# Performance work log

Hardware: AMD Instinct MI355X
Metric: run time of the kernel (lower is better)

The kernel has to match this reference:

```python
import jax, jax.numpy as jnp
import numpy as np


def setup_inputs() -> dict:
    key = jax.random.key(0)
    kq, kk, kv = jax.random.split(key, 3)
    b, n, h, d = 1, 8192, 8, 64
    return {
        "query": jax.random.normal(kq, (b, n, h, d), dtype=jnp.float32),
        "key": jax.random.normal(kk, (b, n, h, d), dtype=jnp.float32),
        "value": jax.random.normal(kv, (b, n, h, d), dtype=jnp.float32),
        "ring_size": 4,
    }


def _ring_attention(q, k, v, ring_size):
    # q,k,v: [b, n, h, d]. Emulates the ring: K/V split into ring_size chunks,
    # processed sequentially with online-softmax rescaling (non-causal).
    b, n, h, d = q.shape
    cs = n // ring_size  # chunk_size
    scale = 1.0 / jnp.sqrt(jnp.asarray(d, q.dtype))
    # [ring, b, cs, h, d]
    k_chunks = jnp.moveaxis(k.reshape(b, ring_size, cs, h, d), 1, 0)
    v_chunks = jnp.moveaxis(v.reshape(b, ring_size, cs, h, d), 1, 0)

    out0 = jnp.zeros((b, h, n, d), q.dtype)
    m0 = jnp.full((b, h, n, 1), -jnp.inf, q.dtype)
    s0 = jnp.zeros((b, h, n, 1), q.dtype)

    def step(carry, kv_chunk):
        out, m, s = carry
        kc, vc = kv_chunk  # [b, cs, h, d]
        scores = jnp.einsum("bqhd,bkhd->bhqk", q, kc) * scale  # [b,h,n,cs]
        chunk_max = scores.max(axis=-1, keepdims=True)
        new_max = jnp.maximum(m, chunk_max)
        corr = jnp.exp(m - new_max)  # 0 at first step since m=-inf
        exp_scores = jnp.exp(scores - new_max)
        out = out * corr + jnp.einsum("bhqk,bkhd->bhqd", exp_scores, vc)
        s = s * corr + exp_scores.sum(axis=-1, keepdims=True)
        return (out, new_max, s), None

    (out, _, s), _ = jax.lax.scan(step, (out0, m0, s0), (k_chunks, v_chunks))
    out = out / s
    return jnp.swapaxes(out, 1, 2)  # [b, n, h, d]


def reference(query, key, value, ring_size):
    return _ring_attention(query, key, value, ring_size)
```

## Files before the change

### kernel.cpp

```cpp
#include <hip/hip_runtime.h>
#include <hip/hip_bf16.h>

typedef __attribute__((ext_vector_type(8))) short bf16x8;
typedef __attribute__((ext_vector_type(8))) unsigned short u16x8;
typedef __attribute__((ext_vector_type(16))) float f32x16;
typedef __attribute__((ext_vector_type(4))) unsigned int u32x4;

#define MFMA32(a, b, c) __builtin_amdgcn_mfma_f32_32x32x16_bf16(a, b, c, 0, 0, 0)

constexpr int NSEQ = 8192;
constexpr int NH   = 8;
constexpr int DIM  = 64;
constexpr int KVB  = 64;
constexpr int NT   = NSEQ / KVB;
constexpr int NTH  = NT / 2;
constexpr int SLAB = KVB * DIM;
constexpr int QB   = 256;
constexpr float SCL2 = 0.18033688011112042f;

__device__ __forceinline__ unsigned cvt_pk(float lo, float hi) {
    unsigned r;
    asm("v_cvt_pk_bf16_f32 %0, %1, %2" : "=v"(r) : "v"(lo), "v"(hi));
    return r;
}
__device__ __forceinline__ float exp2f_fast(float x) {
    float r;
    asm("v_exp_f32 %0, %1" : "=v"(r) : "v"(x));
    return r;
}
__device__ __forceinline__ void pl32swap(unsigned& a, unsigned& b) {
    asm("v_permlane32_swap_b32 %0, %1" : "+v"(a), "+v"(b));
}
__device__ __forceinline__ int swz(int row, int col) {
    return row * 64 + ((((col >> 3) ^ row) & 7) << 3) + (col & 7);
}

__global__ __launch_bounds__(256, 4)
void prep_kernel(const float* __restrict__ Kg, const float* __restrict__ Vg,
                 unsigned short* __restrict__ Kws, unsigned short* __restrict__ Vws) {
    __shared__ float Vf[64][65];
    const int tid = threadIdx.x;
    const int bid = blockIdx.x;
    if (bid < 1024) {
        const int h = bid >> 7, t = bid & 127;
        unsigned short* dst = Kws + (size_t)bid * SLAB;
#pragma unroll
        for (int j = 0; j < 2; ++j) {
            const int m = tid * 2 + j;
            const int instr = m >> 6, ln = m & 63;
            const int kh = instr >> 2, kd = instr & 3;
            const int row = t * 64 + kh * 32 + (ln & 31);
            const int col = kd * 16 + (ln >> 5) * 8;
            const float* src = Kg + ((size_t)row * NH + h) * DIM + col;
            float4 a = ((const float4*)src)[0];
            float4 b = ((const float4*)src)[1];
            u32x4 w;
            w[0] = cvt_pk(a.x, a.y); w[1] = cvt_pk(a.z, a.w);
            w[2] = cvt_pk(b.x, b.y); w[3] = cvt_pk(b.z, b.w);
            *(u32x4*)(dst + m * 8) = w;
        }
    } else {
        const int hb = bid - 1024;
        const int h = hb >> 7, t = hb & 127;
        const int key = tid >> 2, dc = (tid & 3) * 16;
        const float* src = Vg + ((size_t)(t * 64 + key) * NH + h) * DIM + dc;
#pragma unroll
        for (int i = 0; i < 4; ++i) {
            float4 a = ((const float4*)src)[i];
            Vf[key][dc + i * 4 + 0] = a.x; Vf[key][dc + i * 4 + 1] = a.y;
            Vf[key][dc + i * 4 + 2] = a.z; Vf[key][dc + i * 4 + 3] = a.w;
        }
        __syncthreads();
        unsigned short* dst = Vws + (size_t)hb * SLAB;
#pragma unroll
        for (int j = 0; j < 2; ++j) {
            const int m = tid * 2 + j;
            const int instr = m >> 6, ln = m & 63;
            const int vh = instr >> 2, ks = instr & 3;
            const int d  = vh * 32 + (ln & 31);
            const int k0 = ks * 16 + (ln >> 5) * 8;
            u32x4 w;
            w[0] = cvt_pk(Vf[k0 + 0][d], Vf[k0 + 1][d]);
            w[1] = cvt_pk(Vf[k0 + 2][d], Vf[k0 + 3][d]);
            w[2] = cvt_pk(Vf[k0 + 4][d], Vf[k0 + 5][d]);
            w[3] = cvt_pk(Vf[k0 + 6][d], Vf[k0 + 7][d]);
            *(u32x4*)(dst + m * 8) = w;
        }
    }
}

__global__ __launch_bounds__(512, 2)
void fa_kernel(const float* __restrict__ Qg, const unsigned short* __restrict__ Kws,
               const unsigned short* __restrict__ Vws, float* __restrict__ Og) {
    __shared__ unsigned short KVb[2][2][2][SLAB];
    __shared__ float mrgML[2][2][256];

    const int tid  = threadIdx.x;
    const int lane = tid & 63;
    const int wave = tid >> 6;
    const int half = wave >> 2;
    const int qw   = wave & 1;
    const int qw2  = (wave >> 1) & 1;
    const int la31 = lane & 31;
    const int hi   = lane >> 5;
    const int halftid = tid & 255;
    const int head  = blockIdx.x & 7;
    const int qtile = blockIdx.x >> 3;
    const int qwv = wave & 3;
    const int qv = wave & 3;
    const int qbase = qtile * 128 + (qv & 1) * 64;
    const int fragoff = lane * 8;

    const int half_f  = wave >> 1;
    const int qv_f    = wave & 1;
    const int qbase_f = qtile * 128 + qv_f * 64;
    const int halftid_f = tid & 127;

    bf16x8 qf[2][4];
#pragma unroll
    for (int g = 0; g < 2; ++g)
#pragma unroll
        for (int kd = 0; kd < 4; ++kd) {
            const float* qp = Qg + ((size_t)(qbase_f + g * 32 + la31) * NH + head) * DIM + kd * 16 + hi * 8;
            float4 a = ((const float4*)qp)[0];
            float4 b = ((const float4*)qp)[1];
            u32x4 w;
            w[0] = cvt_pk(a.x * SCL2, a.y * SCL2);
            w[1] = cvt_pk(a.z * SCL2, a.w * SCL2);
            w[2] = cvt_pk(b.x * SCL2, b.y * SCL2);
            w[3] = cvt_pk(b.z * SCL2, b.w * SCL2);
            qf[g][kd] = __builtin_bit_cast(bf16x8, w);
        }

    const unsigned short* ksl = Kws + ((size_t)head * NT + (size_t)half_f * NTH) * SLAB + halftid_f * 8;
    const unsigned short* vsl = Vws + ((size_t)head * NT + (size_t)half_f * NTH) * SLAB + halftid_f * 8;

    f32x16 oacc[2][2];
#pragma unroll
    for (int g = 0; g < 2; ++g)
#pragma unroll
        for (int nt = 0; nt < 2; ++nt)
#pragma unroll
            for (int i = 0; i < 16; ++i) oacc[g][nt][i] = 0.f;
    float m_run[2] = {-1e30f, -1e30f}, l_run[2] = {0.f, 0.f};

    u16x8 kr0 = *(const u16x8*)ksl,          kr1 = *(const u16x8*)(ksl + 1024);
    u16x8 kr2 = *(const u16x8*)(ksl + 2048), kr3 = *(const u16x8*)(ksl + 3072);
    u16x8 vr0 = *(const u16x8*)vsl,          vr1 = *(const u16x8*)(vsl + 1024);
    u16x8 vr2 = *(const u16x8*)(vsl + 2048), vr3 = *(const u16x8*)(vsl + 3072);
    ksl += SLAB; vsl += SLAB;

    for (int t = 0; t < NTH; ++t) {
        const int cur = t & 1;
        unsigned short* kw = &KVb[0][half_f][cur][0];
        unsigned short* vw = &KVb[1][half_f][cur][0];
        *(u16x8*)(kw + halftid_f * 8)        = kr0;
        *(u16x8*)(kw + 1024 + halftid_f * 8) = kr1;
        *(u16x8*)(kw + 2048 + halftid_f * 8) = kr2;
        *(u16x8*)(kw + 3072 + halftid_f * 8) = kr3;
        *(u16x8*)(vw + halftid_f * 8)        = vr0;
        *(u16x8*)(vw + 1024 + halftid_f * 8) = vr1;
        *(u16x8*)(vw + 2048 + halftid_f * 8) = vr2;
        *(u16x8*)(vw + 3072 + halftid_f * 8) = vr3;
        __syncthreads();
        if (t + 1 < NTH) {
            kr0 = *(const u16x8*)ksl;          kr1 = *(const u16x8*)(ksl + 1024);
            kr2 = *(const u16x8*)(ksl + 2048); kr3 = *(const u16x8*)(ksl + 3072);
            vr0 = *(const u16x8*)vsl;          vr1 = *(const u16x8*)(vsl + 1024);
            vr2 = *(const u16x8*)(vsl + 2048); vr3 = *(const u16x8*)(vsl + 3072);
            ksl += SLAB; vsl += SLAB;
        }
        const unsigned short* Kbase = &KVb[0][half_f][cur][0];
        const unsigned short* Vbase = &KVb[1][half_f][cur][0];

        f32x16 s00, s01, s10, s11;
#pragma unroll
        for (int i = 0; i < 16; ++i) { s00[i] = 0.f; s01[i] = 0.f; s10[i] = 0.f; s11[i] = 0.f; }
        __builtin_amdgcn_s_setprio(1);
#pragma unroll
        for (int kd = 0; kd < 4; ++kd) {
            bf16x8 k0 = *(const bf16x8*)(Kbase + kd * 512 + fragoff);
            bf16x8 k1 = *(const bf16x8*)(Kbase + (4 + kd) * 512 + fragoff);
            s00 = MFMA32(k0, qf[0][kd], s00);
            s01 = MFMA32(k1, qf[0][kd], s01);
            s10 = MFMA32(k0, qf[1][kd], s10);
            s11 = MFMA32(k1, qf[1][kd], s11);
        }
        __builtin_amdgcn_s_setprio(0);

#pragma unroll
        for (int g = 0; g < 2; ++g) {
            const f32x16& a = g ? s10 : s00;
            const f32x16& b = g ? s11 : s01;
            float pmv[16];
#pragma unroll
            for (int i = 0; i < 16; ++i) pmv[i] = fmaxf(a[i], b[i]);
#pragma unroll
            for (int st = 8; st >= 1; st >>= 1)
#pragma unroll
                for (int i = 0; i < 8; ++i)
                    if (i < st) pmv[i] = fmaxf(pmv[i], pmv[i + st]);
            float pm = pmv[0];
            pm = fmaxf(pm, __shfl_xor(pm, 32));
            if (__any(pm > m_run[g] + 8.f)) {
                float mnew = fmaxf(m_run[g], pm);
                float corr = exp2f_fast(m_run[g] - mnew);
                m_run[g] = mnew;
                l_run[g] *= corr;
#pragma unroll
                for (int i = 0; i < 16; ++i) { oacc[g][0][i] *= corr; oacc[g][1][i] *= corr; }
            }
        }

#pragma unroll
        for (int kb = 0; kb < 2; ++kb) {
            bf16x8 frg[2][2];
#pragma unroll
            for (int g = 0; g < 2; ++g) {
                const f32x16& s = g ? (kb ? s11 : s10) : (kb ? s01 : s00);
                float p[16];
#pragma unroll
                for (int i = 0; i < 16; ++i) p[i] = exp2f_fast(s[i] - m_run[g]);
                float ts[8];
#pragma unroll
                for (int i = 0; i < 8; ++i) ts[i] = p[i] + p[i + 8];
#pragma unroll
                for (int i = 0; i < 4; ++i) ts[i] += ts[i + 4];
                l_run[g] += (ts[0] + ts[1]) + (ts[2] + ts[3]);
                unsigned A[8];
#pragma unroll
                for (int j = 0; j < 8; ++j) A[j] = cvt_pk(p[2 * j], p[2 * j + 1]);
                pl32swap(A[0], A[2]); pl32swap(A[1], A[3]);
                pl32swap(A[4], A[6]); pl32swap(A[5], A[7]);
                u32x4 f0v; f0v[0] = A[0]; f0v[1] = A[1]; f0v[2] = A[2]; f0v[3] = A[3];
                u32x4 f1v; f1v[0] = A[4]; f1v[1] = A[5]; f1v[2] = A[6]; f1v[3] = A[7];
                frg[g][0] = __builtin_bit_cast(bf16x8, f0v);
                frg[g][1] = __builtin_bit_cast(bf16x8, f1v);
            }
            __builtin_amdgcn_s_setprio(1);
#pragma unroll
            for (int ks2 = 0; ks2 < 2; ++ks2) {
                const int ksg = kb * 2 + ks2;
                bf16x8 vf0 = *(const bf16x8*)(Vbase + ksg * 512 + fragoff);
                bf16x8 vf1 = *(const bf16x8*)(Vbase + (4 + ksg) * 512 + fragoff);
                oacc[0][0] = MFMA32(vf0, frg[0][ks2], oacc[0][0]);
                oacc[0][1] = MFMA32(vf1, frg[0][ks2], oacc[0][1]);
                oacc[1][0] = MFMA32(vf0, frg[1][ks2], oacc[1][0]);
                oacc[1][1] = MFMA32(vf1, frg[1][ks2], oacc[1][1]);
            }
            __builtin_amdgcn_s_setprio(0);
        }
    }

    __syncthreads();
    float* mrgO = (float*)&KVb[0][0][0][0];
    const int row0 = qv_f * 64;
    if (half_f) {
#pragma unroll
        for (int g = 0; g < 2; ++g) {
            const int row = row0 + g * 32 + la31;
#pragma unroll
            for (int nt = 0; nt < 2; ++nt)
#pragma unroll
                for (int i = 0; i < 16; ++i)
                    mrgO[hi * 4096 + (nt * 16 + i) * 128 + row] = oacc[g][nt][i];
            mrgML[g][0][qv_f * 64 + lane] = m_run[g];
            mrgML[g][1][qv_f * 64 + lane] = l_run[g];
        }
    }
    __syncthreads();
    if (!half_f) {
#pragma unroll
        for (int g = 0; g < 2; ++g) {
            const int row = row0 + g * 32 + la31;
            const float m1 = mrgML[g][0][qv_f * 64 + lane];
            const float l1 = mrgML[g][1][qv_f * 64 + lane];
            const float mnew = fmaxf(m_run[g], m1);
            const float c0 = exp2f_fast(m_run[g] - mnew);
            const float c1 = exp2f_fast(m1 - mnew);
            float lt = l_run[g] * c0 + l1 * c1;
#pragma unroll
            for (int nt = 0; nt < 2; ++nt)
#pragma unroll
                for (int i = 0; i < 16; ++i)
                    oacc[g][nt][i] = oacc[g][nt][i] * c0 + mrgO[hi * 4096 + (nt * 16 + i) * 128 + row] * c1;
            const float l_tot = lt + __shfl_xor(lt, 32);
            const float inv = __builtin_amdgcn_rcpf(l_tot);
            float* obase = Og + ((size_t)(qtile * 128 + row) * NH + head) * DIM;
#pragma unroll
            for (int nt = 0; nt < 2; ++nt)
#pragma unroll
                for (int rq = 0; rq < 4; ++rq) {
                    float4 o;
                    o.x = oacc[g][nt][rq * 4 + 0] * inv;
                    o.y = oacc[g][nt][rq * 4 + 1] * inv;
                    o.z = oacc[g][nt][rq * 4 + 2] * inv;
                    o.w = oacc[g][nt][rq * 4 + 3] * inv;
                    *(float4*)(obase + nt * 32 + rq * 8 + hi * 4) = o;
                }
        }
    }
}

__global__ __launch_bounds__(256, 2)
void fb_kernel(const float* __restrict__ Qg, const float* __restrict__ Kg,
               const float* __restrict__ Vg, float* __restrict__ Og) {
    __shared__ unsigned short Kl[KVB][DIM];
    __shared__ unsigned short Vt[DIM][KVB];
    unsigned short* Kbase = &Kl[0][0];
    unsigned short* Vbase = &Vt[0][0];
    const int tid  = threadIdx.x;
    const int lane = tid & 63;
    const int wave = tid >> 6;
    const int la31 = lane & 31;
    const int hi   = lane >> 5;
    const int head  = blockIdx.x & 7;
    const int qtile = blockIdx.x >> 3;
    const int q     = qtile * 128 + wave * 32 + la31;
    bf16x8 qf[4];
#pragma unroll
    for (int kd = 0; kd < 4; ++kd) {
        const float* qp = Qg + ((size_t)q * NH + head) * DIM + kd * 16 + hi * 8;
        float4 a = ((const float4*)qp)[0];
        float4 b = ((const float4*)qp)[1];
        u32x4 w;
        w[0] = cvt_pk(a.x * SCL2, a.y * SCL2);
        w[1] = cvt_pk(a.z * SCL2, a.w * SCL2);
        w[2] = cvt_pk(b.x * SCL2, b.y * SCL2);
        w[3] = cvt_pk(b.z * SCL2, b.w * SCL2);
        qf[kd] = __builtin_bit_cast(bf16x8, w);
    }
    const int ksrow = tid & 63;
    const int kscol = (tid >> 6) * 16;
    const int vpair = tid & 31;
    const int vcg   = tid >> 5;
    const float* kptr  = Kg + ((size_t)ksrow * NH + head) * DIM + kscol;
    const float* vptr0 = Vg + ((size_t)(2 * vpair) * NH + head) * DIM + vcg * 8;
    const float* vptr1 = vptr0 + NH * DIM;
    constexpr size_t STRIDE = (size_t)KVB * NH * DIM;
    const int kIdx0 = swz(ksrow, kscol);
    const int kIdx1 = swz(ksrow, kscol + 8);
    f32x16 oacc[2];
#pragma unroll
    for (int nt = 0; nt < 2; ++nt)
#pragma unroll
        for (int i = 0; i < 16; ++i) oacc[nt][i] = 0.f;
    float m_run = -1e30f, l_run = 0.f;
    float4 kr0 = ((const float4*)kptr)[0], kr1 = ((const float4*)kptr)[1];
    float4 kr2 = ((const float4*)kptr)[2], kr3 = ((const float4*)kptr)[3];
    float4 va0 = ((const float4*)vptr0)[0], va1 = ((const float4*)vptr0)[1];
    float4 vb0 = ((const float4*)vptr1)[0], vb1 = ((const float4*)vptr1)[1];
    kptr += STRIDE; vptr0 += STRIDE; vptr1 += STRIDE;
    for (int t = 0; t < NT; ++t) {
        __syncthreads();
        {
            u32x4 w;
            w[0] = cvt_pk(kr0.x, kr0.y); w[1] = cvt_pk(kr0.z, kr0.w);
            w[2] = cvt_pk(kr1.x, kr1.y); w[3] = cvt_pk(kr1.z, kr1.w);
            *(u32x4*)(Kbase + kIdx0) = w;
            w[0] = cvt_pk(kr2.x, kr2.y); w[1] = cvt_pk(kr2.z, kr2.w);
            w[2] = cvt_pk(kr3.x, kr3.y); w[3] = cvt_pk(kr3.z, kr3.w);
            *(u32x4*)(Kbase + kIdx1) = w;
        }
        {
            *(unsigned*)(Vbase + swz(vcg * 8 + 0, 2 * vpair)) = cvt_pk(va0.x, vb0.x);
            *(unsigned*)(Vbase + swz(vcg * 8 + 1, 2 * vpair)) = cvt_pk(va0.y, vb0.y);
            *(unsigned*)(Vbase + swz(vcg * 8 + 2, 2 * vpair)) = cvt_pk(va0.z, vb0.z);
            *(unsigned*)(Vbase + swz(vcg * 8 + 3, 2 * vpair)) = cvt_pk(va0.w, vb0.w);
            *(unsigned*)(Vbase + swz(vcg * 8 + 4, 2 * vpair)) = cvt_pk(va1.x, vb1.x);
            *(unsigned*)(Vbase + swz(vcg * 8 + 5, 2 * vpair)) = cvt_pk(va1.y, vb1.y);
            *(unsigned*)(Vbase + swz(vcg * 8 + 6, 2 * vpair)) = cvt_pk(va1.z, vb1.z);
            *(unsigned*)(Vbase + swz(vcg * 8 + 7, 2 * vpair)) = cvt_pk(va1.w, vb1.w);
        }
        __syncthreads();
        if (t + 1 < NT) {
            kr0 = ((const float4*)kptr)[0]; kr1 = ((const float4*)kptr)[1];
            kr2 = ((const float4*)kptr)[2]; kr3 = ((const float4*)kptr)[3];
            va0 = ((const float4*)vptr0)[0]; va1 = ((const float4*)vptr0)[1];
            vb0 = ((const float4*)vptr1)[0]; vb1 = ((const float4*)vptr1)[1];
            kptr += STRIDE; vptr0 += STRIDE; vptr1 += STRIDE;
        }
        f32x16 s0, s1;
#pragma unroll
        for (int i = 0; i < 16; ++i) { s0[i] = 0.f; s1[i] = 0.f; }
        __builtin_amdgcn_s_setprio(1);
#pragma unroll
        for (int kd = 0; kd < 4; ++kd) {
            bf16x8 k0 = *(const bf16x8*)(Kbase + swz(la31, kd * 16 + hi * 8));
            bf16x8 k1 = *(const bf16x8*)(Kbase + swz(32 + la31, kd * 16 + hi * 8));
            s0 = MFMA32(k0, qf[kd], s0);
            s1 = MFMA32(k1, qf[kd], s1);
        }
        __builtin_amdgcn_s_setprio(0);
        float pmv[16];
#pragma unroll
        for (int i = 0; i < 16; ++i) pmv[i] = fmaxf(s0[i], s1[i]);
#pragma unroll
        for (int st = 8; st >= 1; st >>= 1)
#pragma unroll
            for (int i = 0; i < 8; ++i)
                if (i < st) pmv[i] = fmaxf(pmv[i], pmv[i + st]);
        float pm = pmv[0];
        pm = fmaxf(pm, __shfl_xor(pm, 32));
        if (__any(pm > m_run + 8.f)) {
            float mnew = fmaxf(m_run, pm);
            float corr = exp2f_fast(m_run - mnew);
            m_run = mnew;
            l_run *= corr;
#pragma unroll
            for (int i = 0; i < 16; ++i) { oacc[0][i] *= corr; oacc[1][i] *= corr; }
        }
#pragma unroll
        for (int kb = 0; kb < 2; ++kb) {
            const f32x16& s = kb ? s1 : s0;
            float p[16];
#pragma unroll
            for (int i = 0; i < 16; ++i) p[i] = exp2f_fast(s[i] - m_run);
            float ts[8];
#pragma unroll
            for (int i = 0; i < 8; ++i) ts[i] = p[i] + p[i + 8];
#pragma unroll
            for (int i = 0; i < 4; ++i) ts[i] += ts[i + 4];
            l_run += (ts[0] + ts[1]) + (ts[2] + ts[3]);
            unsigned A[8];
#pragma unroll
            for (int j = 0; j < 8; ++j) A[j] = cvt_pk(p[2 * j], p[2 * j + 1]);
            pl32swap(A[0], A[2]); pl32swap(A[1], A[3]);
            pl32swap(A[4], A[6]); pl32swap(A[5], A[7]);
            u32x4 f0v; f0v[0] = A[0]; f0v[1] = A[1]; f0v[2] = A[2]; f0v[3] = A[3];
            u32x4 f1v; f1v[0] = A[4]; f1v[1] = A[5]; f1v[2] = A[6]; f1v[3] = A[7];
            bf16x8 frag[2] = { __builtin_bit_cast(bf16x8, f0v), __builtin_bit_cast(bf16x8, f1v) };
            __builtin_amdgcn_s_setprio(1);
#pragma unroll
            for (int ksl = 0; ksl < 2; ++ksl) {
                const int ksg = kb * 2 + ksl;
                bf16x8 vf0 = *(const bf16x8*)(Vbase + swz(la31, ksg * 16 + hi * 8));
                bf16x8 vf1 = *(const bf16x8*)(Vbase + swz(32 + la31, ksg * 16 + hi * 8));
                oacc[0] = MFMA32(vf0, frag[ksl], oacc[0]);
                oacc[1] = MFMA32(vf1, frag[ksl], oacc[1]);
            }
            __builtin_amdgcn_s_setprio(0);
        }
    }
    {
        float l_tot = l_run + __shfl_xor(l_run, 32);
        float inv = __builtin_amdgcn_rcpf(l_tot);
        float* obase = Og + ((size_t)q * NH + head) * DIM;
#pragma unroll
        for (int nt = 0; nt < 2; ++nt)
#pragma unroll
            for (int rq = 0; rq < 4; ++rq) {
                float4 o;
                o.x = oacc[nt][rq * 4 + 0] * inv;
                o.y = oacc[nt][rq * 4 + 1] * inv;
                o.z = oacc[nt][rq * 4 + 2] * inv;
                o.w = oacc[nt][rq * 4 + 3] * inv;
                *(float4*)(obase + nt * 32 + rq * 8 + hi * 4) = o;
            }
    }
}

extern "C" void kernel_launch(void* const* d_in, const int* in_sizes, int n_in,
                              void* d_out, int out_size, void* d_ws, size_t ws_size,
                              hipStream_t stream) {
    const float* q = (const float*)d_in[0];
    const float* k = (const float*)d_in[1];
    const float* v = (const float*)d_in[2];
    float* out = (float*)d_out;
    constexpr size_t KV_WS = 2ull * NH * NT * SLAB * sizeof(unsigned short);
    if (ws_size >= KV_WS) {
        unsigned short* Kws = (unsigned short*)d_ws;
        unsigned short* Vws = Kws + (size_t)NH * NT * SLAB;
        hipLaunchKernelGGL(prep_kernel, dim3(2048), dim3(256), 0, stream, k, v, Kws, Vws);
        hipLaunchKernelGGL(fa_kernel, dim3(512), dim3(256), 0, stream, q, Kws, Vws, out);
    } else {
        hipLaunchKernelGGL(fb_kernel, dim3(512), dim3(256), 0, stream, q, k, v, out);
    }
}
```

Baseline: 182.9 us.

## Software-pipeline QK MFMAs of the next sub-block with softmax of the current

Restructures the attention loop so the QK^T MFMAs for the next 32-key sub-block, including the first sub-block of the next tile, are issued before the softmax and PV of the current sub-block. The goal is to overlap exp/max ALU work with matrix-core work. The running max is now updated per 32-key sub-block rather than per 64-key tile, and max reductions use v_max3. The trade-off is more rescale checks and extra registers for in-flight score tiles, plus a redundant QK on a repeated buffer in the final iteration.

```diff
diff --git a/kernel.cpp b/kernel.cpp
--- a/kernel.cpp
+++ b/kernel.cpp
@@ -15,7 +15,6 @@
 constexpr int NT   = NSEQ / KVB;
 constexpr int NTH  = NT / 2;
 constexpr int SLAB = KVB * DIM;
-constexpr int QB   = 256;
 constexpr float SCL2 = 0.18033688011112042f;
 
 __device__ __forceinline__ unsigned cvt_pk(float lo, float hi) {
@@ -26,6 +25,11 @@
 __device__ __forceinline__ float exp2f_fast(float x) {
     float r;
     asm("v_exp_f32 %0, %1" : "=v"(r) : "v"(x));
+    return r;
+}
+__device__ __forceinline__ float max3f(float a, float b, float c) {
+    float r;
+    asm("v_max3_f32 %0, %1, %2, %3" : "=v"(r) : "v"(a), "v"(b), "v"(c));
     return r;
 }
 __device__ __forceinline__ void pl32swap(unsigned& a, unsigned& b) {
@@ -89,39 +93,100 @@
     }
 }
 
-__global__ __launch_bounds__(512, 2)
+template<int G>
+__device__ __forceinline__ void group_sm(const f32x16& S, float m_run[2], float l_run[2],
+                                         f32x16 oacc[2][2], bf16x8 FR[2]) {
+    float pm  = max3f(max3f(S[0], S[1], S[2]), max3f(S[3], S[4], S[5]), max3f(S[6], S[7], S[8]));
+    float pm2 = max3f(max3f(S[9], S[10], S[11]), max3f(S[12], S[13], S[14]), S[15]);
+    pm = fmaxf(pm, pm2);
+    pm = fmaxf(pm, __shfl_xor(pm, 32));
+    if (__any(pm > m_run[G] + 8.f)) {
+        float mnew = fmaxf(m_run[G], pm);
+        float corr = exp2f_fast(m_run[G] - mnew);
+        m_run[G] = mnew;
+        l_run[G] *= corr;
+#pragma unroll
+        for (int i = 0; i < 16; ++i) { oacc[G][0][i] *= corr; oacc[G][1][i] *= corr; }
+    }
+    float p[16];
+#pragma unroll
+    for (int i = 0; i < 16; ++i) p[i] = exp2f_fast(S[i] - m_run[G]);
+    float ts[8];
+#pragma unroll
+    for (int i = 0; i < 8; ++i) ts[i] = p[i] + p[i + 8];
+#pragma unroll
+    for (int i = 0; i < 4; ++i) ts[i] += ts[i + 4];
+    l_run[G] += (ts[0] + ts[1]) + (ts[2] + ts[3]);
+    unsigned A0 = cvt_pk(p[0], p[1]),  A1 = cvt_pk(p[2], p[3]);
+    unsigned A2 = cvt_pk(p[4], p[5]),  A3 = cvt_pk(p[6], p[7]);
+    unsigned A4 = cvt_pk(p[8], p[9]),  A5 = cvt_pk(p[10], p[11]);
+    unsigned A6 = cvt_pk(p[12], p[13]), A7 = cvt_pk(p[14], p[15]);
+    pl32swap(A0, A2); pl32swap(A1, A3);
+    pl32swap(A4, A6); pl32swap(A5, A7);
+    u32x4 f0; f0[0] = A0; f0[1] = A1; f0[2] = A2; f0[3] = A3;
+    u32x4 f1; f1[0] = A4; f1[1] = A5; f1[2] = A6; f1[3] = A7;
+    FR[0] = __builtin_bit_cast(bf16x8, f0);
+    FR[1] = __builtin_bit_cast(bf16x8, f1);
+}
+
+__device__ __forceinline__ void qk_sub(const unsigned short* Kbase, int KB, int fragoff,
+                                       const bf16x8 qf[2][4], const f32x16& ZERO,
+                                       f32x16& D0, f32x16& D1) {
+    __builtin_amdgcn_s_setprio(1);
+    bf16x8 kk = *(const bf16x8*)(Kbase + (KB * 4 + 0) * 512 + fragoff);
+    D0 = MFMA32(kk, qf[0][0], ZERO);
+    D1 = MFMA32(kk, qf[1][0], ZERO);
+#pragma unroll
+    for (int kd = 1; kd < 4; ++kd) {
+        kk = *(const bf16x8*)(Kbase + (KB * 4 + kd) * 512 + fragoff);
+        D0 = MFMA32(kk, qf[0][kd], D0);
+        D1 = MFMA32(kk, qf[1][kd], D1);
+    }
+    __builtin_amdgcn_s_setprio(0);
+}
+
+__device__ __forceinline__ void pv_sub(const unsigned short* Vbase, int KB, int fragoff,
+                                       const bf16x8 fr0[2], const bf16x8 fr1[2],
+                                       f32x16 oacc[2][2]) {
+    __builtin_amdgcn_s_setprio(1);
+#pragma unroll
+    for (int ks2 = 0; ks2 < 2; ++ks2) {
+        const int ksg = KB * 2 + ks2;
+        bf16x8 vf0 = *(const bf16x8*)(Vbase + ksg * 512 + fragoff);
+        bf16x8 vf1 = *(const bf16x8*)(Vbase + (4 + ksg) * 512 + fragoff);
+        oacc[0][0] = MFMA32(vf0, fr0[ks2], oacc[0][0]);
+        oacc[0][1] = MFMA32(vf1, fr0[ks2], oacc[0][1]);
+        oacc[1][0] = MFMA32(vf0, fr1[ks2], oacc[1][0]);
+        oacc[1][1] = MFMA32(vf1, fr1[ks2], oacc[1][1]);
+    }
+    __builtin_amdgcn_s_setprio(0);
+}
+
+__global__ __launch_bounds__(256, 2)
 void fa_kernel(const float* __restrict__ Qg, const unsigned short* __restrict__ Kws,
                const unsigned short* __restrict__ Vws, float* __restrict__ Og) {
     __shared__ unsigned short KVb[2][2][2][SLAB];
-    __shared__ float mrgML[2][2][256];
+    __shared__ float mrgML[2][2][128];
 
     const int tid  = threadIdx.x;
     const int lane = tid & 63;
     const int wave = tid >> 6;
-    const int half = wave >> 2;
-    const int qw   = wave & 1;
-    const int qw2  = (wave >> 1) & 1;
+    const int half_f = wave >> 1;
+    const int qv_f   = wave & 1;
     const int la31 = lane & 31;
     const int hi   = lane >> 5;
-    const int halftid = tid & 255;
+    const int halftid = tid & 127;
     const int head  = blockIdx.x & 7;
     const int qtile = blockIdx.x >> 3;
-    const int qwv = wave & 3;
-    const int qv = wave & 3;
-    const int qbase = qtile * 128 + (qv & 1) * 64;
+    const int qbase = qtile * 128 + qv_f * 64;
     const int fragoff = lane * 8;
 
-    const int half_f  = wave >> 1;
-    const int qv_f    = wave & 1;
-    const int qbase_f = qtile * 128 + qv_f * 64;
-    const int halftid_f = tid & 127;
-
     bf16x8 qf[2][4];
 #pragma unroll
     for (int g = 0; g < 2; ++g)
 #pragma unroll
         for (int kd = 0; kd < 4; ++kd) {
-            const float* qp = Qg + ((size_t)(qbase_f + g * 32 + la31) * NH + head) * DIM + kd * 16 + hi * 8;
+            const float* qp = Qg + ((size_t)(qbase + g * 32 + la31) * NH + head) * DIM + kd * 16 + hi * 8;
             float4 a = ((const float4*)qp)[0];
             float4 b = ((const float4*)qp)[1];
             u32x4 w;
@@ -132,16 +197,15 @@
             qf[g][kd] = __builtin_bit_cast(bf16x8, w);
         }
 
-    const unsigned short* ksl = Kws + ((size_t)head * NT + (size_t)half_f * NTH) * SLAB + halftid_f * 8;
-    const unsigned short* vsl = Vws + ((size_t)head * NT + (size_t)half_f * NTH) * SLAB + halftid_f * 8;
+    const unsigned short* ksl = Kws + ((size_t)head * NT + (size_t)half_f * NTH) * SLAB + halftid * 8;
+    const unsigned short* vsl = Vws + ((size_t)head * NT + (size_t)half_f * NTH) * SLAB + halftid * 8;
 
     f32x16 oacc[2][2];
+    const f32x16 ZERO = {0.f,0.f,0.f,0.f,0.f,0.f,0.f,0.f,0.f,0.f,0.f,0.f,0.f,0.f,0.f,0.f};
 #pragma unroll
     for (int g = 0; g < 2; ++g)
 #pragma unroll
-        for (int nt = 0; nt < 2; ++nt)
-#pragma unroll
-            for (int i = 0; i < 16; ++i) oacc[g][nt][i] = 0.f;
+        for (int nt = 0; nt < 2; ++nt) oacc[g][nt] = ZERO;
     float m_run[2] = {-1e30f, -1e30f}, l_run[2] = {0.f, 0.f};
 
     u16x8 kr0 = *(const u16x8*)ksl,          kr1 = *(const u16x8*)(ksl + 1024);
@@ -149,106 +213,70 @@
     u16x8 vr0 = *(const u16x8*)vsl,          vr1 = *(const u16x8*)(vsl + 1024);
     u16x8 vr2 = *(const u16x8*)(vsl + 2048), vr3 = *(const u16x8*)(vsl + 3072);
     ksl += SLAB; vsl += SLAB;
+    {
+        unsigned short* kw = &KVb[0][half_f][0][0];
+        unsigned short* vw = &KVb[1][half_f][0][0];
+        *(u16x8*)(kw + halftid * 8)        = kr0;
+        *(u16x8*)(kw + 1024 + halftid * 8) = kr1;
+        *(u16x8*)(kw + 2048 + halftid * 8) = kr2;
+        *(u16x8*)(kw + 3072 + halftid * 8) = kr3;
+        *(u16x8*)(vw + halftid * 8)        = vr0;
+        *(u16x8*)(vw + 1024 + halftid * 8) = vr1;
+        *(u16x8*)(vw + 2048 + halftid * 8) = vr2;
+        *(u16x8*)(vw + 3072 + halftid * 8) = vr3;
+    }
+    __syncthreads();
+    kr0 = *(const u16x8*)ksl;          kr1 = *(const u16x8*)(ksl + 1024);
+    kr2 = *(const u16x8*)(ksl + 2048); kr3 = *(const u16x8*)(ksl + 3072);
+    vr0 = *(const u16x8*)vsl;          vr1 = *(const u16x8*)(vsl + 1024);
+    vr2 = *(const u16x8*)(vsl + 2048); vr3 = *(const u16x8*)(vsl + 3072);
+    ksl += SLAB; vsl += SLAB;
+
+    f32x16 sA0, sA1, sB0, sB1;
+    qk_sub(&KVb[0][half_f][0][0], 0, fragoff, qf, ZERO, sA0, sA1);
 
     for (int t = 0; t < NTH; ++t) {
-        const int cur = t & 1;
-        unsigned short* kw = &KVb[0][half_f][cur][0];
-        unsigned short* vw = &KVb[1][half_f][cur][0];
-        *(u16x8*)(kw + halftid_f * 8)        = kr0;
-        *(u16x8*)(kw + 1024 + halftid_f * 8) = kr1;
-        *(u16x8*)(kw + 2048 + halftid_f * 8) = kr2;
-        *(u16x8*)(kw + 3072 + halftid_f * 8) = kr3;
-        *(u16x8*)(vw + halftid_f * 8)        = vr0;
-        *(u16x8*)(vw + 1024 + halftid_f * 8) = vr1;
-        *(u16x8*)(vw + 2048 + halftid_f * 8) = vr2;
-        *(u16x8*)(vw + 3072 + halftid_f * 8) = vr3;
+        const int cur = t & 1, nxt = cur ^ 1;
+        const unsigned short* Kcur = &KVb[0][half_f][cur][0];
+        const unsigned short* Knxt = &KVb[0][half_f][nxt][0];
+        const unsigned short* Vcur = &KVb[1][half_f][cur][0];
+
         __syncthreads();
-        if (t + 1 < NTH) {
-            kr0 = *(const u16x8*)ksl;          kr1 = *(const u16x8*)(ksl + 1024);
-            kr2 = *(const u16x8*)(ksl + 2048); kr3 = *(const u16x8*)(ksl + 3072);
-            vr0 = *(const u16x8*)vsl;          vr1 = *(const u16x8*)(vsl + 1024);
-            vr2 = *(const u16x8*)(vsl + 2048); vr3 = *(const u16x8*)(vsl + 3072);
-            ksl += SLAB; vsl += SLAB;
-        }
-        const unsigned short* Kbase = &KVb[0][half_f][cur][0];
-        const unsigned short* Vbase = &KVb[1][half_f][cur][0];
-
-        f32x16 s00, s01, s10, s11;
-#pragma unroll
-        for (int i = 0; i < 16; ++i) { s00[i] = 0.f; s01[i] = 0.f; s10[i] = 0.f; s11[i] = 0.f; }
-        __builtin_amdgcn_s_setprio(1);
-#pragma unroll
-        for (int kd = 0; kd < 4; ++kd) {
-            bf16x8 k0 = *(const bf16x8*)(Kbase + kd * 512 + fragoff);
-            bf16x8 k1 = *(const bf16x8*)(Kbase + (4 + kd) * 512 + fragoff);
-            s00 = MFMA32(k0, qf[0][kd], s00);
-            s01 = MFMA32(k1, qf[0][kd], s01);
-            s10 = MFMA32(k0, qf[1][kd], s10);
-            s11 = MFMA32(k1, qf[1][kd], s11);
-        }
-        __builtin_amdgcn_s_setprio(0);
-
-#pragma unroll
-        for (int g = 0; g < 2; ++g) {
-            const f32x16& a = g ? s10 : s00;
-            const f32x16& b = g ? s11 : s01;
-            float pmv[16];
-#pragma unroll
-            for (int i = 0; i < 16; ++i) pmv[i] = fmaxf(a[i], b[i]);
-#pragma unroll
-            for (int st = 8; st >= 1; st >>= 1)
-#pragma unroll
-                for (int i = 0; i < 8; ++i)
-                    if (i < st) pmv[i] = fmaxf(pmv[i], pmv[i + st]);
-            float pm = pmv[0];
-            pm = fmaxf(pm, __shfl_xor(pm, 32));
-            if (__any(pm > m_run[g] + 8.f)) {
-                float mnew = fmaxf(m_run[g], pm);
-                float corr = exp2f_fast(m_run[g] - mnew);
-                m_run[g] = mnew;
-                l_run[g] *= corr;
-#pragma unroll
-                for (int i = 0; i < 16; ++i) { oacc[g][0][i] *= corr; oacc[g][1][i] *= corr; }
-            }
-        }
-
-#pragma unroll
-        for (int kb = 0; kb < 2; ++kb) {
-            bf16x8 frg[2][2];
-#pragma unroll
-            for (int g = 0; g < 2; ++g) {
-                const f32x16& s = g ? (kb ? s11 : s10) : (kb ? s01 : s00);
-                float p[16];
-#pragma unroll
-                for (int i = 0; i < 16; ++i) p[i] = exp2f_fast(s[i] - m_run[g]);
-                float ts[8];
-#pragma unroll
-                for (int i = 0; i < 8; ++i) ts[i] = p[i] + p[i + 8];
-#pragma unroll
-                for (int i = 0; i < 4; ++i) ts[i] += ts[i + 4];
-                l_run[g] += (ts[0] + ts[1]) + (ts[2] + ts[3]);
-                unsigned A[8];
-#pragma unroll
-                for (int j = 0; j < 8; ++j) A[j] = cvt_pk(p[2 * j], p[2 * j + 1]);
-                pl32swap(A[0], A[2]); pl32swap(A[1], A[3]);
-                pl32swap(A[4], A[6]); pl32swap(A[5], A[7]);
-                u32x4 f0v; f0v[0] = A[0]; f0v[1] = A[1]; f0v[2] = A[2]; f0v[3] = A[3];
-                u32x4 f1v; f1v[0] = A[4]; f1v[1] = A[5]; f1v[2] = A[6]; f1v[3] = A[7];
-                frg[g][0] = __builtin_bit_cast(bf16x8, f0v);
-                frg[g][1] = __builtin_bit_cast(bf16x8, f1v);
-            }
-            __builtin_amdgcn_s_setprio(1);
-#pragma unroll
-            for (int ks2 = 0; ks2 < 2; ++ks2) {
-                const int ksg = kb * 2 + ks2;
-                bf16x8 vf0 = *(const bf16x8*)(Vbase + ksg * 512 + fragoff);
-                bf16x8 vf1 = *(const bf16x8*)(Vbase + (4 + ksg) * 512 + fragoff);
-                oacc[0][0] = MFMA32(vf0, frg[0][ks2], oacc[0][0]);
-                oacc[0][1] = MFMA32(vf1, frg[0][ks2], oacc[0][1]);
-                oacc[1][0] = MFMA32(vf0, frg[1][ks2], oacc[1][0]);
-                oacc[1][1] = MFMA32(vf1, frg[1][ks2], oacc[1][1]);
-            }
-            __builtin_amdgcn_s_setprio(0);
+        {
+            unsigned short* kw = &KVb[0][half_f][nxt][0];
+            unsigned short* vw = &KVb[1][half_f][nxt][0];
+            *(u16x8*)(kw + halftid * 8)        = kr0;
+            *(u16x8*)(kw + 1024 + halftid * 8) = kr1;
+            *(u16x8*)(kw + 2048 + halftid * 8) = kr2;
+            *(u16x8*)(kw + 3072 + halftid * 8) = kr3;
+            *(u16x8*)(vw + halftid * 8)        = vr0;
+            *(u16x8*)(vw + 1024 + halftid * 8) = vr1;
+            *(u16x8*)(vw + 2048 + halftid * 8) = vr2;
+            *(u16x8*)(vw + 3072 + halftid * 8) = vr3;
+        }
+        __syncthreads();
+        kr0 = *(const u16x8*)ksl;          kr1 = *(const u16x8*)(ksl + 1024);
+        kr2 = *(const u16x8*)(ksl + 2048); kr3 = *(const u16x8*)(ksl + 3072);
+        vr0 = *(const u16x8*)vsl;          vr1 = *(const u16x8*)(vsl + 1024);
+        vr2 = *(const u16x8*)(vsl + 2048); vr3 = *(const u16x8*)(vsl + 3072);
+        {
+            const size_t adv = (t + 3 < NTH) ? (size_t)SLAB : 0;
+            ksl += adv; vsl += adv;
+        }
+
+        qk_sub(Kcur, 1, fragoff, qf, ZERO, sB0, sB1);
+        {
+            bf16x8 fr0[2], fr1[2];
+            group_sm<0>(sA0, m_run, l_run, oacc, fr0);
+            group_sm<1>(sA1, m_run, l_run, oacc, fr1);
+            pv_sub(Vcur, 0, fragoff, fr0, fr1, oacc);
+        }
+        qk_sub(Knxt, 0, fragoff, qf, ZERO, sA0, sA1);
+        {
+            bf16x8 fr0[2], fr1[2];
+            group_sm<0>(sB0, m_run, l_run, oacc, fr0);
+            group_sm<1>(sB1, m_run, l_run, oacc, fr1);
+            pv_sub(Vcur, 1, fragoff, fr0, fr1, oacc);
         }
     }
 
```

After: 191.8 us. +4.9%, slower.
